# Kernel tuning notes

Hardware: AMD Instinct MI355X
Metric: run time of the kernel (lower is better)

Reference implementation:

```python
import jax, jax.numpy as jnp
import numpy as np

B, S, D = 8, 2048, 512
EPS = float(jnp.finfo(jnp.float32).eps)  # torch RMSNorm eps=None -> finfo eps


def rmsnorm(x, w):
    var = jnp.mean(jnp.square(x), axis=-1, keepdims=True)
    return x * jax.lax.rsqrt(var + EPS) * w


def setup_inputs() -> dict:
    key = jax.random.key(0)
    ks = jax.random.split(key, 9)
    x = jax.random.normal(ks[0], (B, S, D), dtype=jnp.float32)
    q_expl = jax.random.normal(ks[1], (B, S, D), dtype=jnp.float32)
    k_expl = jax.random.normal(ks[2], (B, S, D), dtype=jnp.float32)
    # parameters (torch Linear: y = x @ W^T + b; store W already transposed [in, out])
    sc1 = 1.0 / np.sqrt(D)
    W1 = jax.random.uniform(ks[3], (D, 2 * D), jnp.float32, -sc1, sc1)
    b1 = jax.random.uniform(ks[4], (2 * D,), jnp.float32, -sc1, sc1)
    W2 = jax.random.uniform(ks[5], (D, D), jnp.float32, -sc1, sc1)
    b2 = jax.random.uniform(ks[6], (D,), jnp.float32, -sc1, sc1)
    norm1_w = jnp.ones((D,), jnp.float32)
    norm2_w = jnp.ones((D,), jnp.float32)
    return {"x": x, "q_expl": q_expl, "k_expl": k_expl,
            "W1": W1, "b1": b1, "W2": W2, "b2": b2,
            "norm1_w": norm1_w, "norm2_w": norm2_w}


def reference(x, q_expl, k_expl, W1, b1, W2, b2, norm1_w, norm2_w):
    d = x.shape[-1]
    # single-head attention: scores [B,S,S]
    scores = jnp.einsum('bqd,bkd->bqk', q_expl, k_expl) / jnp.sqrt(jnp.float32(d))
    attn = jax.nn.softmax(scores, axis=-1)
    attn_out = jnp.einsum('bqk,bkd->bqd', attn, x)
    # dropout is identity in eval mode
    h = rmsnorm(x + attn_out, norm1_w)
    # GeGLU FFN: Linear(D->2D), chunk, gelu(x1)*x2, Linear(D->D)
    proj = h @ W1 + b1
    x1, x2 = jnp.split(proj, 2, axis=-1)
    g = jax.nn.gelu(x1, approximate=False) * x2
    ff = g @ W2 + b2
    return rmsnorm(h + ff, norm2_w)
```

## Files before the change

### kernel.cpp

```cpp
#include <hip/hip_runtime.h>
#include <math.h>

static constexpr float EPS_F = 1.1920929e-07f;
static constexpr float SCL   = 0.044194173824159216f;

typedef __attribute__((ext_vector_type(8))) short  short8;
typedef __attribute__((ext_vector_type(4))) float  floatx4;

__device__ __forceinline__ float4 ld4(const float* p){ return *(const float4*)p; }
__device__ __forceinline__ ushort f2bf(float f){
  union { float f; unsigned u; } v; v.f = f;
  return (ushort)((v.u + 0x7FFFu + ((v.u >> 16) & 1u)) >> 16);
}
__device__ __forceinline__ float bf2f(ushort h){
  union { unsigned u; float f; } v; v.u = ((unsigned)h) << 16;
  return v.f;
}
#define MFMA16(A,B,C) __builtin_amdgcn_mfma_f32_16x16x32_bf16((A),(B),(C),0,0,0)

__device__ __forceinline__ void gld16(void* lds, const void* g){
  __builtin_amdgcn_global_load_lds(
      (const __attribute__((address_space(1))) unsigned int*)g,
      (__attribute__((address_space(3))) unsigned int*)lds, 16, 0, 0);
}

__global__ __launch_bounds__(256)
void prep(const float* __restrict__ q, const float* __restrict__ k,
          const float* __restrict__ x, const float* __restrict__ W1,
          const float* __restrict__ W2,
          ushort* __restrict__ Qb, ushort* __restrict__ Kb,
          ushort* __restrict__ XT, ushort* __restrict__ W1T,
          ushort* __restrict__ W2T)
{
  const int bi = blockIdx.x, t = threadIdx.x;
  if (bi < 8192){
    const size_t i4 = ((size_t)bi*256 + t)*4;
    float4 v = ld4(q + i4);
    ushort4 o;
    o.x=f2bf(v.x*SCL); o.y=f2bf(v.y*SCL); o.z=f2bf(v.z*SCL); o.w=f2bf(v.w*SCL);
    *(ushort4*)(Qb + i4) = o;
    float4 u = ld4(k + i4);
    o.x=f2bf(u.x); o.y=f2bf(u.y); o.z=f2bf(u.z); o.w=f2bf(u.w);
    *(ushort4*)(Kb + i4) = o;
    return;
  }
  const float* in; ushort* out; int R, C, c0, r0; size_t boff;
  if (bi < 10240){
    const int id = bi - 8192;
    in = x; out = XT; R = 2048; C = 512;
    boff = (size_t)(id >> 8) * R * C;
    c0 = (id & 7)*64; r0 = ((id >> 3) & 31)*64;
  } else if (bi < 10368){
    const int id = bi - 10240;
    in = W1; out = W1T; R = 512; C = 1024; boff = 0;
    c0 = (id & 15)*64; r0 = (id >> 4)*64;
  } else {
    const int id = bi - 10368;
    in = W2; out = W2T; R = 512; C = 512; boff = 0;
    c0 = (id & 7)*64; r0 = (id >> 3)*64;
  }
  __shared__ __align__(16) ushort tile[64*68];
#pragma unroll
  for (int it = 0; it < 4; ++it){
    int f = t + it*256, r = f >> 4, c4 = f & 15;
    float4 v = ld4(in + boff + (size_t)(r0+r)*C + c0 + c4*4);
    ushort4 o; o.x=f2bf(v.x); o.y=f2bf(v.y); o.z=f2bf(v.z); o.w=f2bf(v.w);
    *(ushort4*)&tile[r*68 + c4*4] = o;
  }
  __syncthreads();
#pragma unroll
  for (int it = 0; it < 4; ++it){
    int f = t + it*256, c = f >> 4, q4 = f & 15;
    ushort4 o;
    o.x = tile[(q4*4+0)*68 + c];
    o.y = tile[(q4*4+1)*68 + c];
    o.z = tile[(q4*4+2)*68 + c];
    o.w = tile[(q4*4+3)*68 + c];
    *(ushort4*)(out + boff + (size_t)(c0+c)*R + r0 + q4*4) = o;
  }
}

__global__ __launch_bounds__(512)
void qk8(const ushort* __restrict__ Qbf, const ushort* __restrict__ Kbf,
         ushort* __restrict__ scores, float* __restrict__ rowsum)
{
  extern __shared__ __align__(16) ushort smem[];
  const int t = threadIdx.x, lane = t & 63, w = t >> 6;
  const int id = blockIdx.x;
  const int b = id & 7, s = id >> 3;
  const int m0 = (s & 7) * 256, n0 = (s >> 3) * 256;
  const ushort* Qb = Qbf + ((size_t)b*2048 + (size_t)m0)*512;
  const ushort* Kb = Kbf + ((size_t)b*2048 + (size_t)n0)*512;
  const int wr = w >> 2, wc = w & 3;
  const int l15 = lane & 15, quad = lane >> 4;
  const int c0  = (quad ^ (l15 & 7)) * 8;
  const int srow = lane >> 3;
  const int skc  = ((lane & 7) ^ srow) * 8;

  floatx4 acc[8][4];
#pragma unroll
  for (int i = 0; i < 8; ++i)
#pragma unroll
    for (int j = 0; j < 4; ++j) acc[i][j] = (floatx4){0.f,0.f,0.f,0.f};

  auto stage = [&](int buf, const ushort* gsrc, int isB, int kt, int h){
    ushort* base = smem + buf*32768 + isB*16384 + h*8192;
#pragma unroll
    for (int r = 0; r < 2; ++r){
      const int rw = r*8 + w;
      gld16(base + rw*512,
            gsrc + (size_t)(h*128 + rw*8 + srow)*512 + kt*64 + skc);
    }
  };

  stage(0, Qb, 0, 0, 0);
  stage(0, Qb, 0, 0, 1);
  stage(0, Kb, 1, 0, 0);
  stage(0, Kb, 1, 0, 1);
  stage(1, Kb, 1, 1, 0);
  stage(1, Kb, 1, 1, 1);
  asm volatile("s_waitcnt vmcnt(4)" ::: "memory");
  __builtin_amdgcn_s_barrier();

  short8 af[2][2], bfr[4][2];
  const int NT = 8;

  for (int kt = 0; kt < NT; ++kt){
    const int cur = kt & 1;
    const ushort* A  = smem + cur*32768;
    const ushort* Bt = A + 16384;
#pragma unroll
    for (int p = 0; p < 4; ++p){
      if (p == 0){
#pragma unroll
        for (int ni = 0; ni < 4; ++ni)
#pragma unroll
          for (int ks = 0; ks < 2; ++ks)
            bfr[ni][ks] = *(const short8*)
              &Bt[(wc*64 + ni*16 + l15)*64 + (c0 ^ (ks*32))];
      }
#pragma unroll
      for (int mi = 0; mi < 2; ++mi)
#pragma unroll
        for (int ks = 0; ks < 2; ++ks)
          af[mi][ks] = *(const short8*)
            &A[(wr*128 + (p*2 + mi)*16 + l15)*64 + (c0 ^ (ks*32))];
      if (p == 0 && kt+1 < NT) stage(cur^1, Qb, 0, kt+1, 0);
      if (p == 1 && kt+1 < NT) stage(cur^1, Qb, 0, kt+1, 1);
      if (p == 2 && kt+2 < NT) stage(cur,   Kb, 1, kt+2, 0);
      if (p == 3 && kt+2 < NT) stage(cur,   Kb, 1, kt+2, 1);
      __builtin_amdgcn_s_barrier();
      asm volatile("s_waitcnt lgkmcnt(0)" ::: "memory");
      __builtin_amdgcn_sched_barrier(0);
      __builtin_amdgcn_s_setprio(1);
#pragma unroll
      for (int mi = 0; mi < 2; ++mi)
#pragma unroll
        for (int ni = 0; ni < 4; ++ni)
#pragma unroll
          for (int ks = 0; ks < 2; ++ks)
            acc[p*2+mi][ni] = MFMA16(af[mi][ks], bfr[ni][ks], acc[p*2+mi][ni]);
      __builtin_amdgcn_s_setprio(0);
      if (p == 3){
        if (kt + 2 < NT) asm volatile("s_waitcnt vmcnt(4)" ::: "memory");
        else             asm volatile("s_waitcnt vmcnt(0)" ::: "memory");
      }
      __builtin_amdgcn_s_barrier();
    }
  }

  ushort* sb = scores + (size_t)b*2048*2048;
#pragma unroll
  for (int m = 0; m < 8; ++m){
    const int rm = m0 + wr*128 + m*16 + quad*4;
    float rs[4] = {0.f,0.f,0.f,0.f};
#pragma unroll
    for (int n = 0; n < 4; ++n){
      const int cn = n0 + wc*64 + n*16 + l15;
#pragma unroll
      for (int r = 0; r < 4; ++r){
        float e = __expf(acc[m][n][r]);
        ushort eb = f2bf(e);
        sb[(size_t)(rm + r)*2048 + cn] = eb;
        rs[r] += bf2f(eb);
      }
    }
#pragma unroll
    for (int r = 0; r < 4; ++r){
      float p2 = rs[r];
      p2 += __shfl_xor(p2, 1); p2 += __shfl_xor(p2, 2);
      p2 += __shfl_xor(p2, 4); p2 += __shfl_xor(p2, 8);
      if (l15 == 0)
        atomicAdd(&rowsum[(size_t)b*2048 + rm + r], p2);
    }
  }
}

__global__ __launch_bounds__(512)
void pv8(const ushort* __restrict__ P, const ushort* __restrict__ XT,
         const float* __restrict__ rowsum, ushort* __restrict__ attn)
{
  extern __shared__ __align__(16) ushort smem[];
  const int t = threadIdx.x, lane = t & 63, w = t >> 6;
  const int id = blockIdx.x;
  const int b = id & 7, s = id >> 3;
  const int m0 = (s >> 2) * 256;
  const int n0 = (s & 3) * 128;
  const ushort* Pb = P  + ((size_t)b*2048 + m0)*2048;
  const ushort* Xb = XT + ((size_t)b*512  + n0)*2048;
  const int wr = w >> 1, wc = w & 1;
  const int l15 = lane & 15, quad = lane >> 4;
  const int c0  = (quad ^ (l15 & 7)) * 8;
  const int srow = lane >> 3;
  const int skc  = ((lane & 7) ^ srow) * 8;

  floatx4 acc[4][4];
#pragma unroll
  for (int i = 0; i < 4; ++i)
#pragma unroll
    for (int j = 0; j < 4; ++j) acc[i][j] = (floatx4){0.f,0.f,0.f,0.f};

  auto stageA = [&](int buf, int kt, int h){
    ushort* base = smem + buf*24576 + h*8192;
#pragma unroll
    for (int r = 0; r < 2; ++r){
      const int rw = r*8 + w;
      gld16(base + rw*512,
            Pb + (size_t)(h*128 + rw*8 + srow)*2048 + kt*64 + skc);
    }
  };
  auto stageB = [&](int buf, int kt){
    ushort* base = smem + buf*24576 + 16384;
#pragma unroll
    for (int r = 0; r < 2; ++r){
      const int rw = r*8 + w;
      gld16(base + rw*512,
            Xb + (size_t)(rw*8 + srow)*2048 + kt*64 + skc);
    }
  };

  stageA(0, 0, 0);
  stageA(0, 0, 1);
  stageB(0, 0);
  stageB(1, 1);
  asm volatile("s_waitcnt vmcnt(2)" ::: "memory");
  __builtin_amdgcn_s_barrier();

  short8 af[2][2], bfr[4][2];
  const int NT = 32;

  for (int kt = 0; kt < NT; ++kt){
    const int cur = kt & 1;
    const ushort* A  = smem + cur*24576;
    const ushort* Bt = A + 16384;

#pragma unroll
    for (int ni = 0; ni < 4; ++ni)
#pragma unroll
      for (int ks = 0; ks < 2; ++ks)
        bfr[ni][ks] = *(const short8*)
          &Bt[(wc*64 + ni*16 + l15)*64 + (c0 ^ (ks*32))];
#pragma unroll
    for (int mi = 0; mi < 2; ++mi)
#pragma unroll
      for (int ks = 0; ks < 2; ++ks)
        af[mi][ks] = *(const short8*)
          &A[(wr*64 + mi*16 + l15)*64 + (c0 ^ (ks*32))];
    if (kt+1 < NT) stageA(cur^1, kt+1, 0);
    __builtin_amdgcn_s_barrier();
    asm volatile("s_waitcnt lgkmcnt(0)" ::: "memory");
    __builtin_amdgcn_sched_barrier(0);
    __builtin_amdgcn_s_setprio(1);
#pragma unroll
    for (int mi = 0; mi < 2; ++mi)
#pragma unroll
      for (int ni = 0; ni < 4; ++ni)
#pragma unroll
        for (int ks = 0; ks < 2; ++ks)
          acc[mi][ni] = MFMA16(af[mi][ks], bfr[ni][ks], acc[mi][ni]);
    __builtin_amdgcn_s_setprio(0);
    __builtin_amdgcn_s_barrier();

#pragma unroll
    for (int mi = 0; mi < 2; ++mi)
#pragma unroll
      for (int ks = 0; ks < 2; ++ks)
        af[mi][ks] = *(const short8*)
          &A[(wr*64 + (2+mi)*16 + l15)*64 + (c0 ^ (ks*32))];
    if (kt+1 < NT) stageA(cur^1, kt+1, 1);
    if (kt+2 < NT) stageB(cur, kt+2);
    __builtin_amdgcn_s_barrier();
    asm volatile("s_waitcnt lgkmcnt(0)" ::: "memory");
    __builtin_amdgcn_sched_barrier(0);
    __builtin_amdgcn_s_setprio(1);
#pragma unroll
    for (int mi = 0; mi < 2; ++mi)
#pragma unroll
      for (int ni = 0; ni < 4; ++ni)
#pragma unroll
        for (int ks = 0; ks < 2; ++ks)
          acc[2+mi][ni] = MFMA16(af[mi][ks], bfr[ni][ks], acc[2+mi][ni]);
    __builtin_amdgcn_s_setprio(0);
    if (kt + 2 < NT) asm volatile("s_waitcnt vmcnt(2)" ::: "memory");
    else             asm volatile("s_waitcnt vmcnt(0)" ::: "memory");
    __builtin_amdgcn_s_barrier();
  }

  ushort* ab = attn + (size_t)b*2048*512;
#pragma unroll
  for (int m = 0; m < 4; ++m){
    const int rm = m0 + wr*64 + m*16 + quad*4;
    float inv[4];
#pragma unroll
    for (int r = 0; r < 4; ++r)
      inv[r] = 1.0f / rowsum[(size_t)b*2048 + rm + r];
#pragma unroll
    for (int n = 0; n < 4; ++n){
      const int cn = n0 + wc*64 + n*16 + l15;
#pragma unroll
      for (int r = 0; r < 4; ++r)
        ab[(size_t)(rm + r)*512 + cn] = f2bf(acc[m][n][r] * inv[r]);
    }
  }
}

__global__ __launch_bounds__(256)
void res_rms1(const float* __restrict__ x, const float* __restrict__ n1w,
              ushort* __restrict__ ah)
{
  const int wid = threadIdx.x >> 6, lane = threadIdx.x & 63;
  const size_t row = (size_t)blockIdx.x*4 + wid;
  ushort* ar = ah + row*512;
  const float* xr = x + row*512;
  ushort4 a0 = *(const ushort4*)&ar[lane*8];
  ushort4 a1 = *(const ushort4*)&ar[lane*8 + 4];
  float4 x0 = ld4(xr + lane*8), x1 = ld4(xr + lane*8 + 4);
  float h[8];
  h[0]=x0.x+bf2f(a0.x); h[1]=x0.y+bf2f(a0.y); h[2]=x0.z+bf2f(a0.z); h[3]=x0.w+bf2f(a0.w);
  h[4]=x1.x+bf2f(a1.x); h[5]=x1.y+bf2f(a1.y); h[6]=x1.z+bf2f(a1.z); h[7]=x1.w+bf2f(a1.w);
  float ss = 0.f;
#pragma unroll
  for (int e=0;e<8;++e) ss += h[e]*h[e];
#pragma unroll
  for (int s=1;s<64;s<<=1) ss += __shfl_xor(ss, s);
  const float rr = rsqrtf(ss*(1.0f/512.0f) + EPS_F);
  ushort4 o0, o1;
  o0.x=f2bf(h[0]*rr*n1w[lane*8+0]); o0.y=f2bf(h[1]*rr*n1w[lane*8+1]);
  o0.z=f2bf(h[2]*rr*n1w[lane*8+2]); o0.w=f2bf(h[3]*rr*n1w[lane*8+3]);
  o1.x=f2bf(h[4]*rr*n1w[lane*8+4]); o1.y=f2bf(h[5]*rr*n1w[lane*8+5]);
  o1.z=f2bf(h[6]*rr*n1w[lane*8+6]); o1.w=f2bf(h[7]*rr*n1w[lane*8+7]);
  *(ushort4*)&ar[lane*8]     = o0;
  *(ushort4*)&ar[lane*8 + 4] = o1;
}

__global__ __launch_bounds__(256)
void ffn1(const ushort* __restrict__ hbf, const ushort* __restrict__ W1T,
          const float* __restrict__ b1, ushort* __restrict__ gbuf)
{
  __shared__ __align__(16) ushort As[2][128*32];
  __shared__ __align__(16) ushort Bs[2][128*32];
  const int t=threadIdx.x, lane=t&63, w=t>>6;
  const int id = blockIdx.x;
  const int xcd = id & 7, sl = id >> 3;
  const int m0 = (xcd*16 + (sl>>3))*128, n0 = (sl & 7)*64;
  const int sr = w*32 + (lane>>2), sc=(lane&3)*8;
  const int ga=(w&1)*4, b2w=(w>>1);
  const int l15=lane&15, quad=lane>>4;
  const int gr0 = (sr < 64) ? (n0+sr) : (448+n0+sr);
  const int sr1 = sr+16;
  const int gr1 = (sr1 < 64) ? (n0+sr1) : (448+n0+sr1);

  floatx4 acc[4][4];
#pragma unroll
  for (int i=0;i<4;++i)
#pragma unroll
    for (int j=0;j<4;++j) acc[i][j]=(floatx4){0.f,0.f,0.f,0.f};

  auto stage = [&](int buf, int k0){
    gld16(&As[buf][(w*32)*32],    hbf + (size_t)(m0+sr)*512  + k0 + sc);
    gld16(&As[buf][(w*32+16)*32], hbf + (size_t)(m0+sr1)*512 + k0 + sc);
    gld16(&Bs[buf][(w*32)*32],    W1T + (size_t)gr0*512 + k0 + sc);
    gld16(&Bs[buf][(w*32+16)*32], W1T + (size_t)gr1*512 + k0 + sc);
  };

  stage(0, 0);
  for (int kc=0; kc<16; ++kc){
    __syncthreads();
    if (kc < 15) stage((kc+1)&1, (kc+1)*32);
    const ushort* A = As[kc&1];
    const ushort* B = Bs[kc&1];
    short8 af[4], bfr[4];
#pragma unroll
    for (int i=0;i<4;++i) af[i] = *(const short8*)&A[((ga+i)*16 + l15)*32 + quad*8];
#pragma unroll
    for (int jj=0;jj<4;++jj){
      const int g1 = (jj<2) ? (b2w*2+jj) : (4 + b2w*2 + (jj-2));
      bfr[jj] = *(const short8*)&B[(g1*16 + l15)*32 + quad*8];
    }
#pragma unroll
    for (int i=0;i<4;++i)
#pragma unroll
      for (int jj=0;jj<4;++jj)
        acc[i][jj] = MFMA16(af[i], bfr[jj], acc[i][jj]);
  }

#pragma unroll
  for (int i=0;i<4;++i){
#pragma unroll
    for (int jj=0;jj<2;++jj){
      const int col = n0 + (b2w*2+jj)*16 + l15;
      const float bb1 = b1[col], bb2 = b1[512+col];
#pragma unroll
      for (int r=0;r<4;++r){
        const int row = m0 + (ga+i)*16 + quad*4 + r;
        float x1 = acc[i][jj][r]   + bb1;
        float x2 = acc[i][jj+2][r] + bb2;
        float gl = 0.5f*x1*(1.0f + erff(x1*0.70710678118654752f));
        gbuf[(size_t)row*512 + col] = f2bf(gl*x2);
      }
    }
  }
}

__global__ __launch_bounds__(256)
void ff128(const ushort* __restrict__ gb, const ushort* __restrict__ W2T,
           ushort* __restrict__ ff)
{
  __shared__ __align__(16) ushort As[2][128*32];
  __shared__ __align__(16) ushort Bs[2][128*32];
  const int t=threadIdx.x, lane=t&63, w=t>>6;
  const int id = blockIdx.x;
  const int xcd = id & 7, sl = id >> 3;
  const int m0 = (xcd*16 + (sl>>2))*128, n0 = (sl & 3)*128;
  const ushort* Ab = gb  + (size_t)m0*512;
  const ushort* Bb = W2T + (size_t)n0*512;
  const int sr = w*32 + (lane>>2), sc = (lane&3)*8;
  const int ga=(w&1)*4, gb2=(w>>1)*4, l15=lane&15, quad=lane>>4;

  floatx4 acc[4][4];
#pragma unroll
  for (int i=0;i<4;++i)
#pragma unroll
    for (int j=0;j<4;++j) acc[i][j]=(floatx4){0.f,0.f,0.f,0.f};

  auto stage = [&](int buf, int k0){
    gld16(&As[buf][(w*32)*32],    Ab + (size_t)sr*512      + k0 + sc);
    gld16(&As[buf][(w*32+16)*32], Ab + (size_t)(sr+16)*512 + k0 + sc);
    gld16(&Bs[buf][(w*32)*32],    Bb + (size_t)sr*512      + k0 + sc);
    gld16(&Bs[buf][(w*32+16)*32], Bb + (size_t)(sr+16)*512 + k0 + sc);
  };

  stage(0, 0);
  for (int kc=0; kc<16; ++kc){
    __syncthreads();
    if (kc < 15) stage((kc+1)&1, (kc+1)*32);
    const ushort* A = As[kc&1];
    const ushort* B = Bs[kc&1];
    short8 af[4], bfr[4];
#pragma unroll
    for (int i=0;i<4;++i) af[i]  = *(const short8*)&A[((ga+i)*16 + l15)*32 + quad*8];
#pragma unroll
    for (int j=0;j<4;++j) bfr[j] = *(const short8*)&B[((gb2+j)*16 + l15)*32 + quad*8];
#pragma unroll
    for (int i=0;i<4;++i)
#pragma unroll
      for (int j=0;j<4;++j)
        acc[i][j] = MFMA16(af[i], bfr[j], acc[i][j]);
  }

#pragma unroll
  for (int i=0;i<4;++i){
    const int rm = m0 + (ga+i)*16 + quad*4;
#pragma unroll
    for (int j=0;j<4;++j){
      const int cn = n0 + (gb2+j)*16 + l15;
#pragma unroll
      for (int r=0;r<4;++r)
        ff[(size_t)(rm+r)*512 + cn] = f2bf(acc[i][j][r]);
    }
  }
}

__global__ __launch_bounds__(256)
void res_rms2(const ushort* __restrict__ hbf, const ushort* __restrict__ ff,
              const float* __restrict__ b2, const float* __restrict__ n2w,
              float* __restrict__ out)
{
  const int wid = threadIdx.x >> 6, lane = threadIdx.x & 63;
  const size_t row = (size_t)blockIdx.x*4 + wid;
  const ushort* hr = hbf + row*512;
  const ushort* fr = ff  + row*512;
  ushort4 h0 = *(const ushort4*)&hr[lane*8];
  ushort4 h1 = *(const ushort4*)&hr[lane*8 + 4];
  ushort4 f0 = *(const ushort4*)&fr[lane*8];
  ushort4 f1 = *(const ushort4*)&fr[lane*8 + 4];
  float4 bb0 = ld4(b2 + lane*8), bb1 = ld4(b2 + lane*8 + 4);
  float y[8];
  y[0]=bf2f(h0.x)+bf2f(f0.x)+bb0.x; y[1]=bf2f(h0.y)+bf2f(f0.y)+bb0.y;
  y[2]=bf2f(h0.z)+bf2f(f0.z)+bb0.z; y[3]=bf2f(h0.w)+bf2f(f0.w)+bb0.w;
  y[4]=bf2f(h1.x)+bf2f(f1.x)+bb1.x; y[5]=bf2f(h1.y)+bf2f(f1.y)+bb1.y;
  y[6]=bf2f(h1.z)+bf2f(f1.z)+bb1.z; y[7]=bf2f(h1.w)+bf2f(f1.w)+bb1.w;
  float ss = 0.f;
#pragma unroll
  for (int e=0;e<8;++e) ss += y[e]*y[e];
#pragma unroll
  for (int s=1;s<64;s<<=1) ss += __shfl_xor(ss, s);
  const float rr = rsqrtf(ss*(1.0f/512.0f) + EPS_F);
  float4 w0 = ld4(n2w + lane*8), w1 = ld4(n2w + lane*8 + 4);
  float* orow = out + row*512;
  float4 o0, o1;
  o0.x=y[0]*rr*w0.x; o0.y=y[1]*rr*w0.y; o0.z=y[2]*rr*w0.z; o0.w=y[3]*rr*w0.w;
  o1.x=y[4]*rr*w1.x; o1.y=y[5]*rr*w1.y; o1.z=y[6]*rr*w1.z; o1.w=y[7]*rr*w1.w;
  *(float4*)(orow + lane*8)     = o0;
  *(float4*)(orow + lane*8 + 4) = o1;
}

extern "C" void kernel_launch(void* const* d_in, const int* in_sizes, int n_in,
                              void* d_out, int out_size, void* d_ws, size_t ws_size,
                              hipStream_t stream)
{
  const float* x   = (const float*)d_in[0];
  const float* q   = (const float*)d_in[1];
  const float* k   = (const float*)d_in[2];
  const float* W1  = (const float*)d_in[3];
  const float* b1  = (const float*)d_in[4];
  const float* W2  = (const float*)d_in[5];
  const float* b2  = (const float*)d_in[6];
  const float* n1w = (const float*)d_in[7];
  const float* n2w = (const float*)d_in[8];
  float* out = (float*)d_out;

  ushort* scoresP = (ushort*)d_ws;
  ushort* XT  = scoresP + (size_t)8*2048*2048;
  ushort* Qbf = XT  + (size_t)8*512*2048;
  ushort* Kbf = Qbf + (size_t)8*2048*512;
  ushort* W1T = Kbf + (size_t)8*2048*512;
  ushort* W2T = W1T + (size_t)1024*512;
  float*  rowsum = (float*)(W2T + (size_t)512*512);
  ushort* attn = Qbf;
  ushort* hbf  = Qbf;
  ushort* gbuf = Kbf;
  ushort* ffb  = scoresP;

  hipMemsetAsync(rowsum, 0, (size_t)8*2048*sizeof(float), stream);
  prep     <<<dim3(10432),  256, 0, stream>>>(q, k, x, W1, W2, Qbf, Kbf, XT, W1T, W2T);
  qk8      <<<dim3(512),    512, 131072, stream>>>(Qbf, Kbf, scoresP, rowsum);
  pv8      <<<dim3(256),    512,  98304, stream>>>(scoresP, XT, rowsum, attn);
  res_rms1 <<<dim3(4096),   256, 0, stream>>>(x, n1w, hbf);
  ffn1     <<<dim3(1024),   256, 0, stream>>>(hbf, W1T, b1, gbuf);
  ff128    <<<dim3(512),    256, 0, stream>>>(gbuf, W2T, ffb);
  res_rms2 <<<dim3(4096),   256, 0, stream>>>(hbf, ffb, b2, n2w, out);
}
```

Before: 315.6 us.

## Retile QK and FFN GEMMs into 256x128 blocks with swizzled K32 pipeline

Replaces the QK score kernel (256x256 tiles, K=64 steps, 128KB LDS) with a 256x128 tile, K=32 step version that uses 48KB LDS and requests 4 blocks per CU. The two FFN GEMMs move from 256-thread 128x128 blocks to 512-thread 256x128 blocks. All three share the new XOR-swizzled LDS layout and a staggered A/B prefetch that splits each K step into two MFMA halves behind barriers. The goal is higher occupancy and fewer bank conflicts, traded against more barriers per unit of work, smaller per-step MFMA batches, and less reuse per QK tile.

```diff
diff --git a/kernel.cpp b/kernel.cpp
--- a/kernel.cpp
+++ b/kernel.cpp
@@ -23,6 +23,7 @@
       (const __attribute__((address_space(1))) unsigned int*)g,
       (__attribute__((address_space(3))) unsigned int*)lds, 16, 0, 0);
 }
+
 
 __global__ __launch_bounds__(256)
 void prep(const float* __restrict__ q, const float* __restrict__ k,
@@ -80,99 +81,98 @@
   }
 }
 
-__global__ __launch_bounds__(512)
-void qk8(const ushort* __restrict__ Qbf, const ushort* __restrict__ Kbf,
+__global__ __launch_bounds__(512, 4)
+void qk2(const ushort* __restrict__ Qbf, const ushort* __restrict__ Kbf,
          ushort* __restrict__ scores, float* __restrict__ rowsum)
 {
   extern __shared__ __align__(16) ushort smem[];
   const int t = threadIdx.x, lane = t & 63, w = t >> 6;
   const int id = blockIdx.x;
   const int b = id & 7, s = id >> 3;
-  const int m0 = (s & 7) * 256, n0 = (s >> 3) * 256;
-  const ushort* Qb = Qbf + ((size_t)b*2048 + (size_t)m0)*512;
-  const ushort* Kb = Kbf + ((size_t)b*2048 + (size_t)n0)*512;
-  const int wr = w >> 2, wc = w & 3;
+  const int m0 = (s & 7) * 256, n0 = (s >> 3) * 128;
+  const ushort* Ab = Qbf + ((size_t)b*2048 + m0)*512;
+  const ushort* Bb = Kbf + ((size_t)b*2048 + n0)*512;
+  const int wr = w >> 1, wc = w & 1;
   const int l15 = lane & 15, quad = lane >> 4;
-  const int c0  = (quad ^ (l15 & 7)) * 8;
-  const int srow = lane >> 3;
-  const int skc  = ((lane & 7) ^ srow) * 8;
-
-  floatx4 acc[8][4];
-#pragma unroll
-  for (int i = 0; i < 8; ++i)
+  const int rl = ((lane >> 2) & 14) | (((lane >> 2) ^ (lane >> 4)) & 1);
+  const int cl = (lane & 3) ^ (rl & 3);
+  const int sw = (l15 & 7) * 8;
+  int aoff[4], boff[4];
+#pragma unroll
+  for (int m = 0; m < 4; ++m)
+    aoff[m] = ((wr*64 + m*16 + l15)*32 + quad*8) ^ sw;
+#pragma unroll
+  for (int n = 0; n < 4; ++n)
+    boff[n] = ((wc*64 + n*16 + l15)*32 + quad*8) ^ sw;
+  const size_t aS0 = (size_t)(w*16 + rl)*512 + cl*8;
+  const size_t aS1 = aS0 + (size_t)128*512;
+  const size_t bS0 = (size_t)(w*16 + rl)*512 + cl*8;
+  const int aD = w*512, bD = 16384 + w*512;
+
+  floatx4 acc[4][4];
+#pragma unroll
+  for (int i = 0; i < 4; ++i)
 #pragma unroll
     for (int j = 0; j < 4; ++j) acc[i][j] = (floatx4){0.f,0.f,0.f,0.f};
 
-  auto stage = [&](int buf, const ushort* gsrc, int isB, int kt, int h){
-    ushort* base = smem + buf*32768 + isB*16384 + h*8192;
-#pragma unroll
-    for (int r = 0; r < 2; ++r){
-      const int rw = r*8 + w;
-      gld16(base + rw*512,
-            gsrc + (size_t)(h*128 + rw*8 + srow)*512 + kt*64 + skc);
-    }
-  };
-
-  stage(0, Qb, 0, 0, 0);
-  stage(0, Qb, 0, 0, 1);
-  stage(0, Kb, 1, 0, 0);
-  stage(0, Kb, 1, 0, 1);
-  stage(1, Kb, 1, 1, 0);
-  stage(1, Kb, 1, 1, 1);
-  asm volatile("s_waitcnt vmcnt(4)" ::: "memory");
+  const int NT = 16;
+  gld16(smem + aD,        Ab + aS0);
+  gld16(smem + 4096 + aD, Ab + aS1);
+  gld16(smem + bD,        Bb + bS0);
+  gld16(smem + 4096 + bD, Bb + bS0 + 32);
+  asm volatile("s_waitcnt vmcnt(1)" ::: "memory");
   __builtin_amdgcn_s_barrier();
 
-  short8 af[2][2], bfr[4][2];
-  const int NT = 8;
-
+  short8 af[2], bfr[4];
   for (int kt = 0; kt < NT; ++kt){
     const int cur = kt & 1;
-    const ushort* A  = smem + cur*32768;
-    const ushort* Bt = A + 16384;
-#pragma unroll
-    for (int p = 0; p < 4; ++p){
-      if (p == 0){
-#pragma unroll
-        for (int ni = 0; ni < 4; ++ni)
-#pragma unroll
-          for (int ks = 0; ks < 2; ++ks)
-            bfr[ni][ks] = *(const short8*)
-              &Bt[(wc*64 + ni*16 + l15)*64 + (c0 ^ (ks*32))];
-      }
-#pragma unroll
-      for (int mi = 0; mi < 2; ++mi)
-#pragma unroll
-        for (int ks = 0; ks < 2; ++ks)
-          af[mi][ks] = *(const short8*)
-            &A[(wr*128 + (p*2 + mi)*16 + l15)*64 + (c0 ^ (ks*32))];
-      if (p == 0 && kt+1 < NT) stage(cur^1, Qb, 0, kt+1, 0);
-      if (p == 1 && kt+1 < NT) stage(cur^1, Qb, 0, kt+1, 1);
-      if (p == 2 && kt+2 < NT) stage(cur,   Kb, 1, kt+2, 0);
-      if (p == 3 && kt+2 < NT) stage(cur,   Kb, 1, kt+2, 1);
-      __builtin_amdgcn_s_barrier();
-      asm volatile("s_waitcnt lgkmcnt(0)" ::: "memory");
-      __builtin_amdgcn_sched_barrier(0);
-      __builtin_amdgcn_s_setprio(1);
-#pragma unroll
-      for (int mi = 0; mi < 2; ++mi)
-#pragma unroll
-        for (int ni = 0; ni < 4; ++ni)
-#pragma unroll
-          for (int ks = 0; ks < 2; ++ks)
-            acc[p*2+mi][ni] = MFMA16(af[mi][ks], bfr[ni][ks], acc[p*2+mi][ni]);
-      __builtin_amdgcn_s_setprio(0);
-      if (p == 3){
-        if (kt + 2 < NT) asm volatile("s_waitcnt vmcnt(4)" ::: "memory");
-        else             asm volatile("s_waitcnt vmcnt(0)" ::: "memory");
-      }
-      __builtin_amdgcn_s_barrier();
-    }
+    const ushort* A  = smem + cur*8192;
+    const ushort* Bt = smem + 16384 + cur*4096;
+#pragma unroll
+    for (int n = 0; n < 4; ++n) bfr[n] = *(const short8*)&Bt[boff[n]];
+#pragma unroll
+    for (int m = 0; m < 2; ++m) af[m] = *(const short8*)&A[aoff[m]];
+    if (kt+1 < NT){
+      ushort* d = smem + (cur^1)*8192;
+      const size_t ko = (size_t)(kt+1)*32;
+      gld16(d + aD,        Ab + aS0 + ko);
+      gld16(d + 4096 + aD, Ab + aS1 + ko);
+    }
+    __builtin_amdgcn_s_barrier();
+    asm volatile("s_waitcnt lgkmcnt(0)" ::: "memory");
+    __builtin_amdgcn_sched_barrier(0);
+    __builtin_amdgcn_s_setprio(1);
+#pragma unroll
+    for (int m = 0; m < 2; ++m)
+#pragma unroll
+      for (int n = 0; n < 4; ++n)
+        acc[m][n] = MFMA16(af[m], bfr[n], acc[m][n]);
+    __builtin_amdgcn_s_setprio(0);
+    __builtin_amdgcn_s_barrier();
+#pragma unroll
+    for (int m = 0; m < 2; ++m) af[m] = *(const short8*)&A[aoff[2+m]];
+    if (kt+2 < NT)
+      gld16(smem + 16384 + cur*4096 + (bD - 16384),
+            Bb + bS0 + (size_t)(kt+2)*32);
+    __builtin_amdgcn_s_barrier();
+    asm volatile("s_waitcnt lgkmcnt(0)" ::: "memory");
+    __builtin_amdgcn_sched_barrier(0);
+    __builtin_amdgcn_s_setprio(1);
+#pragma unroll
+    for (int m = 0; m < 2; ++m)
+#pragma unroll
+      for (int n = 0; n < 4; ++n)
+        acc[2+m][n] = MFMA16(af[m], bfr[n], acc[2+m][n]);
+    __builtin_amdgcn_s_setprio(0);
+    if (kt + 2 < NT) asm volatile("s_waitcnt vmcnt(1)" ::: "memory");
+    else             asm volatile("s_waitcnt vmcnt(0)" ::: "memory");
+    __builtin_amdgcn_s_barrier();
   }
 
   ushort* sb = scores + (size_t)b*2048*2048;
 #pragma unroll
-  for (int m = 0; m < 8; ++m){
-    const int rm = m0 + wr*128 + m*16 + quad*4;
+  for (int m = 0; m < 4; ++m){
+    const int rm = m0 + wr*64 + m*16 + quad*4;
     float rs[4] = {0.f,0.f,0.f,0.f};
 #pragma unroll
     for (int n = 0; n < 4; ++n){
@@ -353,68 +353,106 @@
   *(ushort4*)&ar[lane*8 + 4] = o1;
 }
 
-__global__ __launch_bounds__(256)
-void ffn1(const ushort* __restrict__ hbf, const ushort* __restrict__ W1T,
+__global__ __launch_bounds__(512, 4)
+void ffn2(const ushort* __restrict__ hbf, const ushort* __restrict__ W1T,
           const float* __restrict__ b1, ushort* __restrict__ gbuf)
 {
-  __shared__ __align__(16) ushort As[2][128*32];
-  __shared__ __align__(16) ushort Bs[2][128*32];
-  const int t=threadIdx.x, lane=t&63, w=t>>6;
+  extern __shared__ __align__(16) ushort smem[];
+  const int t = threadIdx.x, lane = t & 63, w = t >> 6;
   const int id = blockIdx.x;
   const int xcd = id & 7, sl = id >> 3;
-  const int m0 = (xcd*16 + (sl>>3))*128, n0 = (sl & 7)*64;
-  const int sr = w*32 + (lane>>2), sc=(lane&3)*8;
-  const int ga=(w&1)*4, b2w=(w>>1);
-  const int l15=lane&15, quad=lane>>4;
-  const int gr0 = (sr < 64) ? (n0+sr) : (448+n0+sr);
-  const int sr1 = sr+16;
-  const int gr1 = (sr1 < 64) ? (n0+sr1) : (448+n0+sr1);
+  const int m0 = (xcd*8 + (sl >> 3)) * 256;
+  const int n0 = (sl & 7) * 64;
+  const ushort* Ab = hbf + (size_t)m0*512;
+  const int wr = w >> 1, wc = w & 1;
+  const int l15 = lane & 15, quad = lane >> 4;
+  const int rl = ((lane >> 2) & 14) | (((lane >> 2) ^ (lane >> 4)) & 1);
+  const int cl = (lane & 3) ^ (rl & 3);
+  const int sw = (l15 & 7) * 8;
+  int aoff[4], boff[4];
+#pragma unroll
+  for (int m = 0; m < 4; ++m)
+    aoff[m] = ((wr*64 + m*16 + l15)*32 + quad*8) ^ sw;
+#pragma unroll
+  for (int n = 0; n < 4; ++n)
+    boff[n] = ((wc*64 + n*16 + l15)*32 + quad*8) ^ sw;
+  const size_t aS0 = (size_t)(w*16 + rl)*512 + cl*8;
+  const size_t aS1 = aS0 + (size_t)128*512;
+  const int br = w*16 + rl;
+  const int bgrow = ((br >> 5) & 1)*512 + n0 + (br >> 6)*32 + (br & 31);
+  const size_t bS0 = (size_t)bgrow*512 + cl*8;
+  const int aD = w*512, bD = 16384 + w*512;
 
   floatx4 acc[4][4];
 #pragma unroll
-  for (int i=0;i<4;++i)
-#pragma unroll
-    for (int j=0;j<4;++j) acc[i][j]=(floatx4){0.f,0.f,0.f,0.f};
-
-  auto stage = [&](int buf, int k0){
-    gld16(&As[buf][(w*32)*32],    hbf + (size_t)(m0+sr)*512  + k0 + sc);
-    gld16(&As[buf][(w*32+16)*32], hbf + (size_t)(m0+sr1)*512 + k0 + sc);
-    gld16(&Bs[buf][(w*32)*32],    W1T + (size_t)gr0*512 + k0 + sc);
-    gld16(&Bs[buf][(w*32+16)*32], W1T + (size_t)gr1*512 + k0 + sc);
-  };
-
-  stage(0, 0);
-  for (int kc=0; kc<16; ++kc){
-    __syncthreads();
-    if (kc < 15) stage((kc+1)&1, (kc+1)*32);
-    const ushort* A = As[kc&1];
-    const ushort* B = Bs[kc&1];
-    short8 af[4], bfr[4];
-#pragma unroll
-    for (int i=0;i<4;++i) af[i] = *(const short8*)&A[((ga+i)*16 + l15)*32 + quad*8];
-#pragma unroll
-    for (int jj=0;jj<4;++jj){
-      const int g1 = (jj<2) ? (b2w*2+jj) : (4 + b2w*2 + (jj-2));
-      bfr[jj] = *(const short8*)&B[(g1*16 + l15)*32 + quad*8];
-    }
-#pragma unroll
-    for (int i=0;i<4;++i)
-#pragma unroll
-      for (int jj=0;jj<4;++jj)
-        acc[i][jj] = MFMA16(af[i], bfr[jj], acc[i][jj]);
-  }
-
-#pragma unroll
-  for (int i=0;i<4;++i){
-#pragma unroll
-    for (int jj=0;jj<2;++jj){
-      const int col = n0 + (b2w*2+jj)*16 + l15;
-      const float bb1 = b1[col], bb2 = b1[512+col];
-#pragma unroll
-      for (int r=0;r<4;++r){
-        const int row = m0 + (ga+i)*16 + quad*4 + r;
-        float x1 = acc[i][jj][r]   + bb1;
-        float x2 = acc[i][jj+2][r] + bb2;
+  for (int i = 0; i < 4; ++i)
+#pragma unroll
+    for (int j = 0; j < 4; ++j) acc[i][j] = (floatx4){0.f,0.f,0.f,0.f};
+
+  const int NT = 16;
+  gld16(smem + aD,        Ab + aS0);
+  gld16(smem + 4096 + aD, Ab + aS1);
+  gld16(smem + bD,        W1T + bS0);
+  gld16(smem + 4096 + bD, W1T + bS0 + 32);
+  asm volatile("s_waitcnt vmcnt(1)" ::: "memory");
+  __builtin_amdgcn_s_barrier();
+
+  short8 af[2], bfr[4];
+  for (int kt = 0; kt < NT; ++kt){
+    const int cur = kt & 1;
+    const ushort* A  = smem + cur*8192;
+    const ushort* Bt = smem + 16384 + cur*4096;
+#pragma unroll
+    for (int n = 0; n < 4; ++n) bfr[n] = *(const short8*)&Bt[boff[n]];
+#pragma unroll
+    for (int m = 0; m < 2; ++m) af[m] = *(const short8*)&A[aoff[m]];
+    if (kt+1 < NT){
+      ushort* d = smem + (cur^1)*8192;
+      const size_t ko = (size_t)(kt+1)*32;
+      gld16(d + aD,        Ab + aS0 + ko);
+      gld16(d + 4096 + aD, Ab + aS1 + ko);
+    }
+    __builtin_amdgcn_s_barrier();
+    asm volatile("s_waitcnt lgkmcnt(0)" ::: "memory");
+    __builtin_amdgcn_sched_barrier(0);
+    __builtin_amdgcn_s_setprio(1);
+#pragma unroll
+    for (int m = 0; m < 2; ++m)
+#pragma unroll
+      for (int n = 0; n < 4; ++n)
+        acc[m][n] = MFMA16(af[m], bfr[n], acc[m][n]);
+    __builtin_amdgcn_s_setprio(0);
+    __builtin_amdgcn_s_barrier();
+#pragma unroll
+    for (int m = 0; m < 2; ++m) af[m] = *(const short8*)&A[aoff[2+m]];
+    if (kt+2 < NT)
+      gld16(smem + cur*4096 + bD, W1T + bS0 + (size_t)(kt+2)*32);
+    __builtin_amdgcn_s_barrier();
+    asm volatile("s_waitcnt lgkmcnt(0)" ::: "memory");
+    __builtin_amdgcn_sched_barrier(0);
+    __builtin_amdgcn_s_setprio(1);
+#pragma unroll
+    for (int m = 0; m < 2; ++m)
+#pragma unroll
+      for (int n = 0; n < 4; ++n)
+        acc[2+m][n] = MFMA16(af[m], bfr[n], acc[2+m][n]);
+    __builtin_amdgcn_s_setprio(0);
+    if (kt + 2 < NT) asm volatile("s_waitcnt vmcnt(1)" ::: "memory");
+    else             asm volatile("s_waitcnt vmcnt(0)" ::: "memory");
+    __builtin_amdgcn_s_barrier();
+  }
+
+#pragma unroll
+  for (int m = 0; m < 4; ++m){
+#pragma unroll
+    for (int n = 0; n < 2; ++n){
+      const int col = n0 + wc*32 + n*16 + l15;
+      const float bb1 = b1[col], bb2 = b1[512 + col];
+#pragma unroll
+      for (int r = 0; r < 4; ++r){
+        const int row = m0 + wr*64 + m*16 + quad*4 + r;
+        float x1 = acc[m][n][r]     + bb1;
+        float x2 = acc[m][n+2][r]   + bb2;
         float gl = 0.5f*x1*(1.0f + erff(x1*0.70710678118654752f));
         gbuf[(size_t)row*512 + col] = f2bf(gl*x2);
       }
@@ -422,61 +460,103 @@
   }
 }
 
-__global__ __launch_bounds__(256)
-void ff128(const ushort* __restrict__ gb, const ushort* __restrict__ W2T,
-           ushort* __restrict__ ff)
-{
-  __shared__ __align__(16) ushort As[2][128*32];
-  __shared__ __align__(16) ushort Bs[2][128*32];
-  const int t=threadIdx.x, lane=t&63, w=t>>6;
+__global__ __launch_bounds__(512, 4)
+void ff2(const ushort* __restrict__ gb, const ushort* __restrict__ W2T,
+         ushort* __restrict__ ff)
+{
+  extern __shared__ __align__(16) ushort smem[];
+  const int t = threadIdx.x, lane = t & 63, w = t >> 6;
   const int id = blockIdx.x;
   const int xcd = id & 7, sl = id >> 3;
-  const int m0 = (xcd*16 + (sl>>2))*128, n0 = (sl & 3)*128;
+  const int m0 = (xcd*8 + (sl >> 2)) * 256;
+  const int n0 = (sl & 3) * 128;
   const ushort* Ab = gb  + (size_t)m0*512;
   const ushort* Bb = W2T + (size_t)n0*512;
-  const int sr = w*32 + (lane>>2), sc = (lane&3)*8;
-  const int ga=(w&1)*4, gb2=(w>>1)*4, l15=lane&15, quad=lane>>4;
+  const int wr = w >> 1, wc = w & 1;
+  const int l15 = lane & 15, quad = lane >> 4;
+  const int rl = ((lane >> 2) & 14) | (((lane >> 2) ^ (lane >> 4)) & 1);
+  const int cl = (lane & 3) ^ (rl & 3);
+  const int sw = (l15 & 7) * 8;
+  int aoff[4], boff[4];
+#pragma unroll
+  for (int m = 0; m < 4; ++m)
+    aoff[m] = ((wr*64 + m*16 + l15)*32 + quad*8) ^ sw;
+#pragma unroll
+  for (int n = 0; n < 4; ++n)
+    boff[n] = ((wc*64 + n*16 + l15)*32 + quad*8) ^ sw;
+  const size_t aS0 = (size_t)(w*16 + rl)*512 + cl*8;
+  const size_t aS1 = aS0 + (size_t)128*512;
+  const size_t bS0 = (size_t)(w*16 + rl)*512 + cl*8;
+  const int aD = w*512, bD = 16384 + w*512;
 
   floatx4 acc[4][4];
 #pragma unroll
-  for (int i=0;i<4;++i)
-#pragma unroll
-    for (int j=0;j<4;++j) acc[i][j]=(floatx4){0.f,0.f,0.f,0.f};
-
-  auto stage = [&](int buf, int k0){
-    gld16(&As[buf][(w*32)*32],    Ab + (size_t)sr*512      + k0 + sc);
-    gld16(&As[buf][(w*32+16)*32], Ab + (size_t)(sr+16)*512 + k0 + sc);
-    gld16(&Bs[buf][(w*32)*32],    Bb + (size_t)sr*512      + k0 + sc);
-    gld16(&Bs[buf][(w*32+16)*32], Bb + (size_t)(sr+16)*512 + k0 + sc);
-  };
-
-  stage(0, 0);
-  for (int kc=0; kc<16; ++kc){
-    __syncthreads();
-    if (kc < 15) stage((kc+1)&1, (kc+1)*32);
-    const ushort* A = As[kc&1];
-    const ushort* B = Bs[kc&1];
-    short8 af[4], bfr[4];
-#pragma unroll
-    for (int i=0;i<4;++i) af[i]  = *(const short8*)&A[((ga+i)*16 + l15)*32 + quad*8];
-#pragma unroll
-    for (int j=0;j<4;++j) bfr[j] = *(const short8*)&B[((gb2+j)*16 + l15)*32 + quad*8];
-#pragma unroll
-    for (int i=0;i<4;++i)
-#pragma unroll
-      for (int j=0;j<4;++j)
-        acc[i][j] = MFMA16(af[i], bfr[j], acc[i][j]);
-  }
-
-#pragma unroll
-  for (int i=0;i<4;++i){
-    const int rm = m0 + (ga+i)*16 + quad*4;
-#pragma unroll
-    for (int j=0;j<4;++j){
-      const int cn = n0 + (gb2+j)*16 + l15;
-#pragma unroll
-      for (int r=0;r<4;++r)
-        ff[(size_t)(rm+r)*512 + cn] = f2bf(acc[i][j][r]);
+  for (int i = 0; i < 4; ++i)
+#pragma unroll
+    for (int j = 0; j < 4; ++j) acc[i][j] = (floatx4){0.f,0.f,0.f,0.f};
+
+  const int NT = 16;
+  gld16(smem + aD,        Ab + aS0);
+  gld16(smem + 4096 + aD, Ab + aS1);
+  gld16(smem + bD,        Bb + bS0);
+  gld16(smem + 4096 + bD, Bb + bS0 + 32);
+  asm volatile("s_waitcnt vmcnt(1)" ::: "memory");
+  __builtin_amdgcn_s_barrier();
+
+  short8 af[2], bfr[4];
+  for (int kt = 0; kt < NT; ++kt){
+    const int cur = kt & 1;
+    const ushort* A  = smem + cur*8192;
+    const ushort* Bt = smem + 16384 + cur*4096;
+#pragma unroll
+    for (int n = 0; n < 4; ++n) bfr[n] = *(const short8*)&Bt[boff[n]];
+#pragma unroll
+    for (int m = 0; m < 2; ++m) af[m] = *(const short8*)&A[aoff[m]];
+    if (kt+1 < NT){
+      ushort* d = smem + (cur^1)*8192;
+      const size_t ko = (size_t)(kt+1)*32;
+      gld16(d + aD,        Ab + aS0 + ko);
+      gld16(d + 4096 + aD, Ab + aS1 + ko);
+    }
+    __builtin_amdgcn_s_barrier();
+    asm volatile("s_waitcnt lgkmcnt(0)" ::: "memory");
+    __builtin_amdgcn_sched_barrier(0);
+    __builtin_amdgcn_s_setprio(1);
+#pragma unroll
+    for (int m = 0; m < 2; ++m)
+#pragma unroll
+      for (int n = 0; n < 4; ++n)
+        acc[m][n] = MFMA16(af[m], bfr[n], acc[m][n]);
+    __builtin_amdgcn_s_setprio(0);
+    __builtin_amdgcn_s_barrier();
+#pragma unroll
+    for (int m = 0; m < 2; ++m) af[m] = *(const short8*)&A[aoff[2+m]];
+    if (kt+2 < NT)
+      gld16(smem + cur*4096 + bD, Bb + bS0 + (size_t)(kt+2)*32);
+    __builtin_amdgcn_s_barrier();
+    asm volatile("s_waitcnt lgkmcnt(0)" ::: "memory");
+    __builtin_amdgcn_sched_barrier(0);
+    __builtin_amdgcn_s_setprio(1);
+#pragma unroll
+    for (int m = 0; m < 2; ++m)
+#pragma unroll
+      for (int n = 0; n < 4; ++n)
+        acc[2+m][n] = MFMA16(af[m], bfr[n], acc[2+m][n]);
+    __builtin_amdgcn_s_setprio(0);
+    if (kt + 2 < NT) asm volatile("s_waitcnt vmcnt(1)" ::: "memory");
+    else             asm volatile("s_waitcnt vmcnt(0)" ::: "memory");
+    __builtin_amdgcn_s_barrier();
+  }
+
+#pragma unroll
+  for (int m = 0; m < 4; ++m){
+    const int rm = m0 + wr*64 + m*16 + quad*4;
+#pragma unroll
+    for (int n = 0; n < 4; ++n){
+      const int cn = n0 + wc*64 + n*16 + l15;
+#pragma unroll
+      for (int r = 0; r < 4; ++r)
+        ff[(size_t)(rm + r)*512 + cn] = f2bf(acc[m][n][r]);
     }
   }
 }
@@ -544,10 +624,10 @@
 
   hipMemsetAsync(rowsum, 0, (size_t)8*2048*sizeof(float), stream);
   prep     <<<dim3(10432),  256, 0, stream>>>(q, k, x, W1, W2, Qbf, Kbf, XT, W1T, W2T);
-  qk8      <<<dim3(512),    512, 131072, stream>>>(Qbf, Kbf, scoresP, rowsum);
-  pv8      <<<dim3(256),    512,  98304, stream>>>(scoresP, XT, rowsum, attn);
+  qk2      <<<dim3(1024),   512, 49152, stream>>>(Qbf, Kbf, scoresP, rowsum);
+  pv8      <<<dim3(256),    512, 98304, stream>>>(scoresP, XT, rowsum, attn);
   res_rms1 <<<dim3(4096),   256, 0, stream>>>(x, n1w, hbf);
-  ffn1     <<<dim3(1024),   256, 0, stream>>>(hbf, W1T, b1, gbuf);
-  ff128    <<<dim3(512),    256, 0, stream>>>(gbuf, W2T, ffb);
+  ffn2     <<<dim3(512),    512, 49152, stream>>>(hbf, W1T, b1, gbuf);
+  ff2      <<<dim3(256),    512, 49152, stream>>>(gbuf, W2T, ffb);
   res_rms2 <<<dim3(4096),   256, 0, stream>>>(hbf, ffb, b2, n2w, out);
 }
```

Measured after the change: 298.0 us. 1.06x faster.
